# Optimization experiments

Measured on AMD Instinct MI355X. Metric: run time of the kernel, lower is better.

Reference implementation:

```python
import jax, jax.numpy as jnp
import numpy as np

N = 50000      # nodes
E = 800000     # edges (avg degree 16)
D = 128        # in_dim == hidden_dim
CD = 3         # coord_dim (SE(3))
L = 3          # num_layers


def setup_inputs() -> dict:
    key = jax.random.key(0)
    ks = jax.random.split(key, 10)
    s = np.float32(1.0 / np.sqrt(D))
    return {
        "x": jax.random.normal(ks[0], (N, D), jnp.float32),
        "pos": jax.random.normal(ks[1], (N, CD), jnp.float32),
        "edge_index": jax.random.randint(ks[2], (2, E), 0, N, dtype=jnp.int32),
        # per-layer stacked params (in_dim == hidden_dim so all layers stack)
        "Wl": jax.random.normal(ks[3], (L, D, D), jnp.float32) * s,
        "bl": jnp.zeros((L, D), jnp.float32),
        "Wc": jax.random.normal(ks[4], (L, D, 1), jnp.float32) * s,
        "bc": jnp.zeros((L, 1), jnp.float32),
        "WR": jax.random.normal(ks[5], (L, D, CD * CD), jnp.float32) * s,
        "bR": jnp.zeros((L, CD * CD), jnp.float32),
        "Wt": jax.random.normal(ks[6], (L, D, CD), jnp.float32) * s,
        "bt": jnp.zeros((L, CD), jnp.float32),
        # final fc
        "Wf": jax.random.normal(ks[7], (D, D), jnp.float32) * s,
        "bf": jnp.zeros((D,), jnp.float32),
    }


def reference(x, pos, edge_index, Wl, bl, Wc, bc, WR, bR, Wt, bt, Wf, bf):
    src, dst = edge_index[0], edge_index[1]
    n = x.shape[0]
    # R defaults to identity, t to zeros (R_dict/t_dict None path)
    R = jnp.broadcast_to(jnp.eye(CD, dtype=x.dtype), (n, CD, CD))
    t = jnp.zeros_like(pos)
    for i in range(L):
        h = x @ Wl[i] + bl[i]                          # (N, D)  per-edge-type linear
        # MessagePassing aggr='add': message x_j = h[src], scatter-add at dst
        out = jax.ops.segment_sum(h[src], dst, num_segments=n)  # (N, D)
        pos = pos + (out @ Wc[i] + bc[i])              # (N,3) + (N,1) broadcast
        R_upd = (out @ WR[i] + bR[i]).reshape(n, CD, CD)
        Q = jnp.linalg.qr(R_upd)[0]                    # orthonormalize rotation update
        R = Q @ R
        t = t + (out @ Wt[i] + bt[i])
        x = out
    z = x @ Wf + bf
    return z, pos, R, t
```

## Files before the change

### kernel.cpp

```cpp
#include <hip/hip_runtime.h>
#include <hip/hip_fp16.h>

typedef _Float16 half8 __attribute__((ext_vector_type(8)));
typedef float floatx4 __attribute__((ext_vector_type(4)));

#define OSH 13
#define BN  128
#define BSH 7

__device__ inline void qr3_q(const double A[3][3], double Q[3][3]){
  double a[3][3];
#pragma unroll
  for (int r = 0; r < 3; r++)
#pragma unroll
    for (int c = 0; c < 3; c++) a[r][c] = A[r][c];

  double v1[3] = {1.0, 0.0, 0.0};
  double tau1 = 0.0;
  {
    double xn2 = a[1][0]*a[1][0] + a[2][0]*a[2][0];
    if (xn2 != 0.0){
      double alpha = a[0][0];
      double beta = -copysign(sqrt(alpha*alpha + xn2), alpha);
      tau1 = (beta - alpha) / beta;
      double inv = 1.0 / (alpha - beta);
      v1[1] = a[1][0] * inv;
      v1[2] = a[2][0] * inv;
#pragma unroll
      for (int c = 1; c < 3; c++){
        double w = a[0][c] + v1[1]*a[1][c] + v1[2]*a[2][c];
        double tw = tau1 * w;
        a[0][c] -= tw;
        a[1][c] -= tw * v1[1];
        a[2][c] -= tw * v1[2];
      }
    }
  }
  double tau2 = 0.0, v2 = 0.0;
  {
    double x2 = a[2][1];
    if (x2 != 0.0){
      double alpha = a[1][1];
      double beta = -copysign(sqrt(alpha*alpha + x2*x2), alpha);
      tau2 = (beta - alpha) / beta;
      v2 = x2 / (alpha - beta);
    }
  }
  double M[3][3] = {{1.0, 0.0, 0.0},
                    {0.0, 1.0 - tau2, -tau2*v2},
                    {0.0, -tau2*v2, 1.0 - tau2*v2*v2}};
#pragma unroll
  for (int c = 0; c < 3; c++){
    double w = v1[0]*M[0][c] + v1[1]*M[1][c] + v1[2]*M[2][c];
#pragma unroll
    for (int r = 0; r < 3; r++)
      Q[r][c] = M[r][c] - tau1 * v1[r] * w;
  }
}

__device__ inline void se3_node_ds(int n, const float ds[13],
                                   const float* __restrict__ bc, const float* __restrict__ bR,
                                   const float* __restrict__ bt, const float* __restrict__ pos_in,
                                   float* __restrict__ pos_o, float* __restrict__ R_o,
                                   float* __restrict__ t_o, int layer){
  double A[3][3], Q[3][3];
#pragma unroll
  for (int r = 0; r < 3; r++)
#pragma unroll
    for (int c = 0; c < 3; c++)
      A[r][c] = (double)ds[1 + r*3 + c] + (double)bR[r*3 + c];
  qr3_q(A, Q);

  double pd = (double)ds[0] + (double)bc[0];
#pragma unroll
  for (int c = 0; c < 3; c++){
    double base = (layer == 0) ? (double)pos_in[n*3 + c] : (double)pos_o[n*3 + c];
    pos_o[n*3 + c] = (float)(base + pd);
  }

  if (layer == 0){
#pragma unroll
    for (int r = 0; r < 3; r++)
#pragma unroll
      for (int c = 0; c < 3; c++)
        R_o[n*9 + r*3 + c] = (float)Q[r][c];
  } else {
    double Rold[3][3];
#pragma unroll
    for (int r = 0; r < 3; r++)
#pragma unroll
      for (int c = 0; c < 3; c++)
        Rold[r][c] = (double)R_o[n*9 + r*3 + c];
#pragma unroll
    for (int r = 0; r < 3; r++)
#pragma unroll
      for (int c = 0; c < 3; c++){
        double s = Q[r][0]*Rold[0][c] + Q[r][1]*Rold[1][c] + Q[r][2]*Rold[2][c];
        R_o[n*9 + r*3 + c] = (float)s;
      }
  }
#pragma unroll
  for (int c = 0; c < 3; c++){
    double base = (layer == 0) ? 0.0 : (double)t_o[n*3 + c];
    t_o[n*3 + c] = (float)(base + (double)ds[10 + c] + (double)bt[c]);
  }
}

__launch_bounds__(256)
__global__ void k_prebin(const float* __restrict__ x, _Float16* __restrict__ o, int N,
                         const float* __restrict__ Wl, const float* __restrict__ Wf,
                         const float* __restrict__ Wc, const float* __restrict__ WR,
                         const float* __restrict__ Wt, _Float16* __restrict__ wTx,
                         _Float16* __restrict__ wHd,
                         const int* __restrict__ src, const int* __restrict__ dst,
                         int E, int nbuck, int capB,
                         int* __restrict__ cursor, int* __restrict__ binned,
                         int cvtB, int prepB){
  __shared__ int cnt[512];
  __shared__ int segbase[512];
  const int b = blockIdx.x;
  const int tid = threadIdx.x;

  if (b < cvtB){
    int c = b*256 + tid;
    if (c >= (N+1)*16) return;
    int n = c >> 4;
    half8 h = {};
    if (n < N){
      const float* p = x + (size_t)c*8;
      float4 f0 = *(const float4*)p;
      float4 f1 = *(const float4*)(p + 4);
      h[0]=(_Float16)f0.x; h[1]=(_Float16)f0.y; h[2]=(_Float16)f0.z; h[3]=(_Float16)f0.w;
      h[4]=(_Float16)f1.x; h[5]=(_Float16)f1.y; h[6]=(_Float16)f1.z; h[7]=(_Float16)f1.w;
    }
    *(half8*)(o + (size_t)c*8) = h;
    return;
  }
  if (b < cvtB + prepB){
    int t = (b - cvtB)*256 + tid;
    if (t < 4*128*128){
      int l = t >> 14;
      int n = (t >> 7) & 127;
      int k = t & 127;
      const float* W = (l < 3) ? (Wl + (size_t)l*16384) : Wf;
      wTx[t] = (_Float16)W[k*128 + n];
    } else if (t < 4*128*128 + 3*16*128){
      int u = t - 4*128*128;
      int l = u >> 11;
      int r = u & 2047;
      int n = r >> 7;
      int k = r & 127;
      float v = 0.f;
      if (n == 0)      v = Wc[(size_t)l*128 + k];
      else if (n < 10) v = WR[(size_t)l*1152 + k*9 + (n-1)];
      else if (n < 13) v = Wt[(size_t)l*384 + k*3 + (n-10)];
      wHd[u] = (_Float16)v;
    }
    return;
  }

  const int bb = b - cvtB - prepB;
  for (int t = tid; t < nbuck; t += 256) cnt[t] = 0;
  __syncthreads();
  const int e0 = bb*4096 + tid;
  int pk[16], bk[16];
#pragma unroll
  for (int j = 0; j < 16; j++){
    int e = e0 + j*256;
    if (e < E){
      int d = dst[e], s = src[e];
      bk[j] = d >> BSH;
      pk[j] = (s << BSH) | (d & (BN-1));
      atomicAdd(&cnt[bk[j]], 1);
    } else bk[j] = -1;
  }
  __syncthreads();
  for (int t = tid; t < nbuck; t += 256){
    int c = cnt[t];
    if (c > 0) segbase[t] = t*capB + atomicAdd(&cursor[t], c);
    cnt[t] = 0;
  }
  __syncthreads();
#pragma unroll
  for (int j = 0; j < 16; j++){
    if (bk[j] >= 0){
      int ord = atomicAdd(&cnt[bk[j]], 1);
      binned[segbase[bk[j]] + ord] = pk[j];
    }
  }
}

__launch_bounds__(256)
__global__ void k_build(const int* __restrict__ binned, const int* __restrict__ cursor,
                        int N, int capB, int capC,
                        int2* __restrict__ sd, int* __restrict__ csr){
  __shared__ int deg2[BN*8];
  __shared__ int lst2[BN*8];
  __shared__ int cnt2[BN*8];
  __shared__ int scn[BN];
  const int b = blockIdx.x, tid = threadIdx.x;
  for (int t = tid; t < BN*8; t += 256){ deg2[t] = 0; cnt2[t] = 0; }
  __syncthreads();
  const int nE = cursor[b];
  const int gbase = b*capB;
  for (int i = tid; i < nE; i += 256){
    int v = binned[gbase + i];
    int s = v >> BSH;
    int o = s >> OSH; if (o > 7) o = 7;
    atomicAdd(&deg2[((v & (BN-1)) << 3) + o], 1);
  }
  __syncthreads();
  int d0 = 0, p0 = 0;
  if (tid < BN){
#pragma unroll
    for (int o = 0; o < 8; o++) d0 += deg2[(tid << 3) + o];
    p0 = (d0+7)&~7;
    scn[tid] = p0;
  }
  __syncthreads();
#pragma unroll
  for (int off = 1; off < BN; off <<= 1){
    int add = 0;
    if (tid < BN && tid >= off) add = scn[tid-off];
    __syncthreads();
    if (tid < BN) scn[tid] += add;
    __syncthreads();
  }
  const int csrb = b*capC;
  int ex = 0;
  if (tid < BN){
    ex = scn[tid] - p0;
    int off0 = ex;
#pragma unroll
    for (int o = 0; o < 8; o++){ lst2[(tid << 3) + o] = off0; off0 += deg2[(tid << 3) + o]; }
    int n0 = b*BN + tid;
    if (n0 < N) sd[n0] = make_int2(csrb + ex, (d0 << 16) | p0);
  }
  __syncthreads();
  for (int i = tid; i < nE; i += 256){
    int v = binned[gbase + i];
    int dl = v & (BN-1), s = v >> BSH;
    int o = s >> OSH; if (o > 7) o = 7;
    int ord = atomicAdd(&cnt2[(dl << 3) + o], 1);
    csr[csrb + lst2[(dl << 3) + o] + ord] = s;
  }
  __syncthreads();
  if (tid < BN){
    for (int j = d0; j < p0; j++) csr[csrb + ex + j] = N;
  }
}

__launch_bounds__(256)
__global__ void k_fused(const _Float16* __restrict__ Xin,
                        const _Float16* __restrict__ Wmain,
                        const _Float16* __restrict__ Whd,
                        const float* __restrict__ bias,
                        const int* __restrict__ csr, const int2* __restrict__ sd,
                        _Float16* __restrict__ Out,
                        int N, int layer,
                        const float* __restrict__ bc, const float* __restrict__ bR,
                        const float* __restrict__ bt, const float* __restrict__ pos_in,
                        float* __restrict__ pos_o, float* __restrict__ R_o,
                        float* __restrict__ t_o){
  __shared__ __align__(16) _Float16 lg[64][136];
  __shared__ __align__(16) float lheads[64*16];
  __shared__ float ldeg[64];

  const int tid  = threadIdx.x;
  const int wave = tid >> 6;
  const int lane = tid & 63;
  const int quad = lane >> 4;
  const int l16  = lane & 15;
  const int rbase0 = blockIdx.x*64;

  {
    const int nbase = rbase0 + wave*16;
    int nn = nbase + (lane & 15);
    int2 sv = (nn < N) ? sd[nn] : make_int2(0, 0);
    const unsigned int* Xu = (const unsigned int*)Xin;
    for (int i = 0; i < 16; i++){
      int s0    = __builtin_amdgcn_readlane(sv.x, i);
      int dpack = __builtin_amdgcn_readlane(sv.y, i);
      int degp  = dpack & 0xffff;
      if (lane == 0) ldeg[wave*16 + i] = (float)(dpack >> 16);
      float acc0 = 0.f, acc1 = 0.f;
      for (int base = 0; base < degp; base += 64){
        int myidx = csr[s0 + base + lane];
        int m = degp - base; m = (m < 64) ? m : 64;
        for (int k = 0; k < m; k += 8){
          unsigned int v[8];
#pragma unroll
          for (int j = 0; j < 8; j++){
            int idx = __builtin_amdgcn_readlane(myidx, k + j);
            v[j] = Xu[(size_t)idx*64 + lane];
          }
#pragma unroll
          for (int j = 0; j < 8; j++){
            float2 f = __half22float2(*(__half2*)&v[j]);
            acc0 += f.x; acc1 += f.y;
          }
        }
      }
      __half2 ho = __floats2half2_rn(acc0, acc1);
      ((unsigned int*)&lg[wave*16 + i][0])[lane] = *(unsigned int*)&ho;
    }
  }
  __syncthreads();

  const int cthi = wave >> 1;
  half8 af[4][2];
#pragma unroll
  for (int kc = 0; kc < 4; kc++)
#pragma unroll
    for (int rt = 0; rt < 2; rt++){
      int rl = (wave & 1)*32 + rt*16 + l16;
      af[kc][rt] = *(const half8*)&lg[rl][kc*32 + quad*8];
    }
  __syncthreads();

  floatx4 acc[2][4] = {};
#pragma unroll
  for (int kc = 0; kc < 4; kc++)
#pragma unroll
    for (int ct = 0; ct < 4; ct++){
      half8 bf = *(const half8*)(Wmain + (size_t)((cthi*4 + ct)*16 + l16)*128 + kc*32 + quad*8);
      acc[0][ct] = __builtin_amdgcn_mfma_f32_16x16x32_f16(af[kc][0], bf, acc[0][ct], 0, 0, 0);
      acc[1][ct] = __builtin_amdgcn_mfma_f32_16x16x32_f16(af[kc][1], bf, acc[1][ct], 0, 0, 0);
    }

#pragma unroll
  for (int rt = 0; rt < 2; rt++){
    float dgv[4];
#pragma unroll
    for (int reg = 0; reg < 4; reg++)
      dgv[reg] = ldeg[(wave & 1)*32 + rt*16 + quad*4 + reg];
#pragma unroll
    for (int ct = 0; ct < 4; ct++){
      int col = (cthi*4 + ct)*16 + l16;
      float b = bias[col];
#pragma unroll
      for (int reg = 0; reg < 4; reg++){
        int rl = (wave & 1)*32 + rt*16 + quad*4 + reg;
        lg[rl][col] = (_Float16)(acc[rt][ct][reg] + b*dgv[reg]);
      }
    }
  }
  __syncthreads();

#pragma unroll
  for (int i = 0; i < 4; i++){
    int idx8 = i*256 + tid;
    int row = idx8 >> 4, c8 = idx8 & 15;
    int gr = rbase0 + row;
    if (gr < N){
      *(half8*)(Out + (size_t)gr*128 + c8*8) = *(const half8*)&lg[row][c8*8];
    } else if (gr == N){
      half8 z = {};
      *(half8*)(Out + (size_t)gr*128 + c8*8) = z;
    }
  }

  {
    floatx4 hacc = {};
#pragma unroll
    for (int kc = 0; kc < 4; kc++){
      half8 ha = *(const half8*)&lg[wave*16 + l16][kc*32 + quad*8];
      half8 bf = *(const half8*)(Whd + (size_t)l16*128 + kc*32 + quad*8);
      hacc = __builtin_amdgcn_mfma_f32_16x16x32_f16(ha, bf, hacc, 0, 0, 0);
    }
#pragma unroll
    for (int reg = 0; reg < 4; reg++)
      lheads[(wave*16 + quad*4 + reg)*16 + l16] = hacc[reg];
  }
  __syncthreads();

  if (tid < 64){
    int n = rbase0 + tid;
    if (n < N){
      float ds[13];
#pragma unroll
      for (int c = 0; c < 13; c++) ds[c] = lheads[tid*16 + c];
      se3_node_ds(n, ds, bc, bR, bt, pos_in, pos_o, R_o, t_o, layer);
    }
  }
}

__launch_bounds__(256)
__global__ void k_fused_fin(const _Float16* __restrict__ Xin,
                        const _Float16* __restrict__ Wmain,
                        const _Float16* __restrict__ Whd,
                        const float* __restrict__ bias,
                        const int* __restrict__ csr, const int2* __restrict__ sd,
                        int N, int layer,
                        const float* __restrict__ bc, const float* __restrict__ bR,
                        const float* __restrict__ bt, const float* __restrict__ pos_in,
                        float* __restrict__ pos_o, float* __restrict__ R_o,
                        float* __restrict__ t_o,
                        const _Float16* __restrict__ Wfin,
                        const float* __restrict__ bfin,
                        float* __restrict__ Zout){
  __shared__ __align__(16) _Float16 lg[64][136];
  __shared__ __align__(16) float lheads[64*16];
  __shared__ float ldeg[64];

  const int tid  = threadIdx.x;
  const int wave = tid >> 6;
  const int lane = tid & 63;
  const int quad = lane >> 4;
  const int l16  = lane & 15;
  const int rbase0 = blockIdx.x*64;

  {
    const int nbase = rbase0 + wave*16;
    int nn = nbase + (lane & 15);
    int2 sv = (nn < N) ? sd[nn] : make_int2(0, 0);
    const unsigned int* Xu = (const unsigned int*)Xin;
    for (int i = 0; i < 16; i++){
      int s0    = __builtin_amdgcn_readlane(sv.x, i);
      int dpack = __builtin_amdgcn_readlane(sv.y, i);
      int degp  = dpack & 0xffff;
      if (lane == 0) ldeg[wave*16 + i] = (float)(dpack >> 16);
      float acc0 = 0.f, acc1 = 0.f;
      for (int base = 0; base < degp; base += 64){
        int myidx = csr[s0 + base + lane];
        int m = degp - base; m = (m < 64) ? m : 64;
        for (int k = 0; k < m; k += 8){
          unsigned int v[8];
#pragma unroll
          for (int j = 0; j < 8; j++){
            int idx = __builtin_amdgcn_readlane(myidx, k + j);
            v[j] = Xu[(size_t)idx*64 + lane];
          }
#pragma unroll
          for (int j = 0; j < 8; j++){
            float2 f = __half22float2(*(__half2*)&v[j]);
            acc0 += f.x; acc1 += f.y;
          }
        }
      }
      __half2 ho = __floats2half2_rn(acc0, acc1);
      ((unsigned int*)&lg[wave*16 + i][0])[lane] = *(unsigned int*)&ho;
    }
  }
  __syncthreads();

  const int cthi = wave >> 1;
  half8 af[4][2];
#pragma unroll
  for (int kc = 0; kc < 4; kc++)
#pragma unroll
    for (int rt = 0; rt < 2; rt++){
      int rl = (wave & 1)*32 + rt*16 + l16;
      af[kc][rt] = *(const half8*)&lg[rl][kc*32 + quad*8];
    }
  __syncthreads();

  floatx4 acc[2][4] = {};
#pragma unroll
  for (int kc = 0; kc < 4; kc++)
#pragma unroll
    for (int ct = 0; ct < 4; ct++){
      half8 bf = *(const half8*)(Wmain + (size_t)((cthi*4 + ct)*16 + l16)*128 + kc*32 + quad*8);
      acc[0][ct] = __builtin_amdgcn_mfma_f32_16x16x32_f16(af[kc][0], bf, acc[0][ct], 0, 0, 0);
      acc[1][ct] = __builtin_amdgcn_mfma_f32_16x16x32_f16(af[kc][1], bf, acc[1][ct], 0, 0, 0);
    }

#pragma unroll
  for (int rt = 0; rt < 2; rt++){
    float dgv[4];
#pragma unroll
    for (int reg = 0; reg < 4; reg++)
      dgv[reg] = ldeg[(wave & 1)*32 + rt*16 + quad*4 + reg];
#pragma unroll
    for (int ct = 0; ct < 4; ct++){
      int col = (cthi*4 + ct)*16 + l16;
      float b = bias[col];
#pragma unroll
      for (int reg = 0; reg < 4; reg++){
        int rl = (wave & 1)*32 + rt*16 + quad*4 + reg;
        lg[rl][col] = (_Float16)(acc[rt][ct][reg] + b*dgv[reg]);
      }
    }
  }
  __syncthreads();

  {
    half8 zf[4][2];
#pragma unroll
    for (int kc = 0; kc < 4; kc++)
#pragma unroll
      for (int rt = 0; rt < 2; rt++){
        int rl = (wave & 1)*32 + rt*16 + l16;
        zf[kc][rt] = *(const half8*)&lg[rl][kc*32 + quad*8];
      }
    floatx4 zacc[2][4] = {};
#pragma unroll
    for (int kc = 0; kc < 4; kc++)
#pragma unroll
      for (int ct = 0; ct < 4; ct++){
        half8 bf = *(const half8*)(Wfin + (size_t)((cthi*4 + ct)*16 + l16)*128 + kc*32 + quad*8);
        zacc[0][ct] = __builtin_amdgcn_mfma_f32_16x16x32_f16(zf[kc][0], bf, zacc[0][ct], 0, 0, 0);
        zacc[1][ct] = __builtin_amdgcn_mfma_f32_16x16x32_f16(zf[kc][1], bf, zacc[1][ct], 0, 0, 0);
      }
#pragma unroll
    for (int rt = 0; rt < 2; rt++)
#pragma unroll
      for (int ct = 0; ct < 4; ct++){
        int col = (cthi*4 + ct)*16 + l16;
        float b = bfin[col];
#pragma unroll
        for (int reg = 0; reg < 4; reg++){
          int gr = rbase0 + (wave & 1)*32 + rt*16 + quad*4 + reg;
          if (gr < N) Zout[(size_t)gr*128 + col] = zacc[rt][ct][reg] + b;
        }
      }
  }

  {
    floatx4 hacc = {};
#pragma unroll
    for (int kc = 0; kc < 4; kc++){
      half8 ha = *(const half8*)&lg[wave*16 + l16][kc*32 + quad*8];
      half8 bf = *(const half8*)(Whd + (size_t)l16*128 + kc*32 + quad*8);
      hacc = __builtin_amdgcn_mfma_f32_16x16x32_f16(ha, bf, hacc, 0, 0, 0);
    }
#pragma unroll
    for (int reg = 0; reg < 4; reg++)
      lheads[(wave*16 + quad*4 + reg)*16 + l16] = hacc[reg];
  }
  __syncthreads();

  if (tid < 64){
    int n = rbase0 + tid;
    if (n < N){
      float ds[13];
#pragma unroll
      for (int c = 0; c < 13; c++) ds[c] = lheads[tid*16 + c];
      se3_node_ds(n, ds, bc, bR, bt, pos_in, pos_o, R_o, t_o, layer);
    }
  }
}

extern "C" void kernel_launch(void* const* d_in, const int* in_sizes, int n_in,
                              void* d_out, int out_size, void* d_ws, size_t ws_size,
                              hipStream_t stream){
  const float* x0  = (const float*)d_in[0];
  const float* pos = (const float*)d_in[1];
  const int*   ei  = (const int*)d_in[2];
  const float* Wl  = (const float*)d_in[3];
  const float* bl  = (const float*)d_in[4];
  const float* Wc  = (const float*)d_in[5];
  const float* bc  = (const float*)d_in[6];
  const float* WR  = (const float*)d_in[7];
  const float* bR  = (const float*)d_in[8];
  const float* Wt  = (const float*)d_in[9];
  const float* bt  = (const float*)d_in[10];
  const float* Wf  = (const float*)d_in[11];
  const float* bf  = (const float*)d_in[12];

  const int N = in_sizes[0] / 128;
  const int E = in_sizes[2] / 2;
  const int* srcp = ei;
  const int* dstp = ei + E;

  float* z_out = (float*)d_out;
  float* pos_o = z_out + (size_t)N*128;
  float* R_o   = pos_o + (size_t)N*3;
  float* t_o   = R_o   + (size_t)N*9;

  const int nbuck = (N + BN - 1) >> BSH;
  const int capB  = (((E + nbuck - 1)/nbuck)*5/4 + 256 + 63) & ~63;
  const int capC  = capB + BN*7;

  char* ws = (char*)d_ws;
  size_t off = 0;
  auto alloc = [&](size_t bytes)->char*{
    char* p = ws + off; off += (bytes + 511) & ~(size_t)511; return p;
  };
  _Float16* bufA = (_Float16*)alloc((size_t)(N+1)*128*2);
  _Float16* bufB = (_Float16*)alloc((size_t)(N+1)*128*2);
  _Float16* wTx  = (_Float16*)alloc((size_t)4*128*128*2);
  _Float16* wHd  = (_Float16*)alloc((size_t)3*16*128*2);
  int2*  sd     = (int2*) alloc((size_t)N*8);
  int*   cursor = (int*)  alloc((size_t)nbuck*4);
  int*   binned = (int*)  alloc((size_t)nbuck*capB*4);
  int*   csr    = (int*)  alloc((size_t)nbuck*capC*4);

  const int cvtB = ((N+1)*16 + 255)/256;
  const int prep_total = 4*128*128 + 3*16*128;
  const int prepB = (prep_total + 255)/256;
  const int binB  = (E + 4095)/4096;

  hipMemsetAsync(cursor, 0, (size_t)nbuck*4, stream);
  k_prebin<<<dim3(cvtB + prepB + binB), dim3(256), 0, stream>>>(
      x0, bufA, N, Wl, Wf, Wc, WR, Wt, wTx, wHd,
      srcp, dstp, E, nbuck, capB, cursor, binned, cvtB, prepB);
  k_build<<<dim3(nbuck), dim3(256), 0, stream>>>(binned, cursor, N, capB, capC, sd, csr);

  const int fused_blocks = (N + 64) >> 6;

  k_fused<<<dim3(fused_blocks), dim3(256), 0, stream>>>(
      bufA, wTx, wHd, bl,
      csr, sd, bufB, N, 0,
      bc, bR, bt, pos, pos_o, R_o, t_o);
  k_fused<<<dim3(fused_blocks), dim3(256), 0, stream>>>(
      bufB, wTx + (size_t)16384, wHd + (size_t)2048, bl + 128,
      csr, sd, bufA, N, 1,
      bc + 1, bR + 9, bt + 3, pos, pos_o, R_o, t_o);
  k_fused_fin<<<dim3(fused_blocks), dim3(256), 0, stream>>>(
      bufA, wTx + (size_t)2*16384, wHd + (size_t)2*2048, bl + 256,
      csr, sd, N, 2,
      bc + 2, bR + 18, bt + 6, pos, pos_o, R_o, t_o,
      wTx + (size_t)3*16384, bf, z_out);
}
```

Measured before the change: 267.9 us.

## Fuse all stages into one cooperative persistent kernel with grid syncs

Replaces the five separate launches (prebin, build, three fused layers) with a single cooperative kernel that loops over work tiles and separates stages with grid-wide barriers. The goal is to remove per-launch overhead and the inter-kernel drain gaps. The cost is that grid size is capped by occupancy, so each block processes several tiles serially, and grid.sync has its own cost. The old multi-kernel path is kept as a fallback if the cooperative launch fails.

```diff
diff --git a/kernel.cpp b/kernel.cpp
--- a/kernel.cpp
+++ b/kernel.cpp
@@ -1,5 +1,8 @@
 #include <hip/hip_runtime.h>
 #include <hip/hip_fp16.h>
+#include <hip/hip_cooperative_groups.h>
+
+namespace cg = cooperative_groups;
 
 typedef _Float16 half8 __attribute__((ext_vector_type(8)));
 typedef float floatx4 __attribute__((ext_vector_type(4)));
@@ -106,60 +109,50 @@
   }
 }
 
-__launch_bounds__(256)
-__global__ void k_prebin(const float* __restrict__ x, _Float16* __restrict__ o, int N,
-                         const float* __restrict__ Wl, const float* __restrict__ Wf,
-                         const float* __restrict__ Wc, const float* __restrict__ WR,
-                         const float* __restrict__ Wt, _Float16* __restrict__ wTx,
-                         _Float16* __restrict__ wHd,
-                         const int* __restrict__ src, const int* __restrict__ dst,
-                         int E, int nbuck, int capB,
-                         int* __restrict__ cursor, int* __restrict__ binned,
-                         int cvtB, int prepB){
-  __shared__ int cnt[512];
-  __shared__ int segbase[512];
-  const int b = blockIdx.x;
+
+__device__ __forceinline__ void dev_cvt_chunk(int c, const float* __restrict__ x,
+                                              _Float16* __restrict__ o, int N){
+  int n = c >> 4;
+  half8 h = {};
+  if (n < N){
+    const float* p = x + (size_t)c*8;
+    float4 f0 = *(const float4*)p;
+    float4 f1 = *(const float4*)(p + 4);
+    h[0]=(_Float16)f0.x; h[1]=(_Float16)f0.y; h[2]=(_Float16)f0.z; h[3]=(_Float16)f0.w;
+    h[4]=(_Float16)f1.x; h[5]=(_Float16)f1.y; h[6]=(_Float16)f1.z; h[7]=(_Float16)f1.w;
+  }
+  *(half8*)(o + (size_t)c*8) = h;
+}
+
+__device__ __forceinline__ void dev_prep_elem(int t,
+    const float* __restrict__ Wl, const float* __restrict__ Wf,
+    const float* __restrict__ Wc, const float* __restrict__ WR,
+    const float* __restrict__ Wt, _Float16* __restrict__ wTx, _Float16* __restrict__ wHd){
+  if (t < 4*128*128){
+    int l = t >> 14;
+    int n = (t >> 7) & 127;
+    int k = t & 127;
+    const float* W = (l < 3) ? (Wl + (size_t)l*16384) : Wf;
+    wTx[t] = (_Float16)W[k*128 + n];
+  } else if (t < 4*128*128 + 3*16*128){
+    int u = t - 4*128*128;
+    int l = u >> 11;
+    int r = u & 2047;
+    int n = r >> 7;
+    int k = r & 127;
+    float v = 0.f;
+    if (n == 0)      v = Wc[(size_t)l*128 + k];
+    else if (n < 10) v = WR[(size_t)l*1152 + k*9 + (n-1)];
+    else if (n < 13) v = Wt[(size_t)l*384 + k*3 + (n-10)];
+    wHd[u] = (_Float16)v;
+  }
+}
+
+__device__ __forceinline__ void dev_bin_block(int bb,
+    const int* __restrict__ src, const int* __restrict__ dst,
+    int E, int nbuck, int capB, int* __restrict__ cursor, int* __restrict__ binned,
+    int* __restrict__ cnt, int* __restrict__ segbase){
   const int tid = threadIdx.x;
-
-  if (b < cvtB){
-    int c = b*256 + tid;
-    if (c >= (N+1)*16) return;
-    int n = c >> 4;
-    half8 h = {};
-    if (n < N){
-      const float* p = x + (size_t)c*8;
-      float4 f0 = *(const float4*)p;
-      float4 f1 = *(const float4*)(p + 4);
-      h[0]=(_Float16)f0.x; h[1]=(_Float16)f0.y; h[2]=(_Float16)f0.z; h[3]=(_Float16)f0.w;
-      h[4]=(_Float16)f1.x; h[5]=(_Float16)f1.y; h[6]=(_Float16)f1.z; h[7]=(_Float16)f1.w;
-    }
-    *(half8*)(o + (size_t)c*8) = h;
-    return;
-  }
-  if (b < cvtB + prepB){
-    int t = (b - cvtB)*256 + tid;
-    if (t < 4*128*128){
-      int l = t >> 14;
-      int n = (t >> 7) & 127;
-      int k = t & 127;
-      const float* W = (l < 3) ? (Wl + (size_t)l*16384) : Wf;
-      wTx[t] = (_Float16)W[k*128 + n];
-    } else if (t < 4*128*128 + 3*16*128){
-      int u = t - 4*128*128;
-      int l = u >> 11;
-      int r = u & 2047;
-      int n = r >> 7;
-      int k = r & 127;
-      float v = 0.f;
-      if (n == 0)      v = Wc[(size_t)l*128 + k];
-      else if (n < 10) v = WR[(size_t)l*1152 + k*9 + (n-1)];
-      else if (n < 13) v = Wt[(size_t)l*384 + k*3 + (n-10)];
-      wHd[u] = (_Float16)v;
-    }
-    return;
-  }
-
-  const int bb = b - cvtB - prepB;
   for (int t = tid; t < nbuck; t += 256) cnt[t] = 0;
   __syncthreads();
   const int e0 = bb*4096 + tid;
@@ -188,17 +181,15 @@
       binned[segbase[bk[j]] + ord] = pk[j];
     }
   }
-}
-
-__launch_bounds__(256)
-__global__ void k_build(const int* __restrict__ binned, const int* __restrict__ cursor,
-                        int N, int capB, int capC,
-                        int2* __restrict__ sd, int* __restrict__ csr){
-  __shared__ int deg2[BN*8];
-  __shared__ int lst2[BN*8];
-  __shared__ int cnt2[BN*8];
-  __shared__ int scn[BN];
-  const int b = blockIdx.x, tid = threadIdx.x;
+  __syncthreads();
+}
+
+__device__ __forceinline__ void dev_build_block(int b,
+    const int* __restrict__ binned, const int* __restrict__ cursor,
+    int N, int capB, int capC, int2* __restrict__ sd, int* __restrict__ csr,
+    int* __restrict__ deg2, int* __restrict__ lst2, int* __restrict__ cnt2,
+    int* __restrict__ scn){
+  const int tid = threadIdx.x;
   for (int t = tid; t < BN*8; t += 256){ deg2[t] = 0; cnt2[t] = 0; }
   __syncthreads();
   const int nE = cursor[b];
@@ -248,30 +239,27 @@
   if (tid < BN){
     for (int j = d0; j < p0; j++) csr[csrb + ex + j] = N;
   }
-}
-
-__launch_bounds__(256)
-__global__ void k_fused(const _Float16* __restrict__ Xin,
-                        const _Float16* __restrict__ Wmain,
-                        const _Float16* __restrict__ Whd,
-                        const float* __restrict__ bias,
-                        const int* __restrict__ csr, const int2* __restrict__ sd,
-                        _Float16* __restrict__ Out,
-                        int N, int layer,
-                        const float* __restrict__ bc, const float* __restrict__ bR,
-                        const float* __restrict__ bt, const float* __restrict__ pos_in,
-                        float* __restrict__ pos_o, float* __restrict__ R_o,
-                        float* __restrict__ t_o){
-  __shared__ __align__(16) _Float16 lg[64][136];
-  __shared__ __align__(16) float lheads[64*16];
-  __shared__ float ldeg[64];
-
+  __syncthreads();
+}
+
+__device__ __forceinline__ void dev_fused_tile(int rbase0,
+    const _Float16* __restrict__ Xin,
+    const _Float16* __restrict__ Wmain, const _Float16* __restrict__ Whd,
+    const float* __restrict__ bias,
+    const int* __restrict__ csr, const int2* __restrict__ sd,
+    _Float16* __restrict__ Out, int N, int layer,
+    const float* __restrict__ bc, const float* __restrict__ bR,
+    const float* __restrict__ bt, const float* __restrict__ pos_in,
+    float* __restrict__ pos_o, float* __restrict__ R_o, float* __restrict__ t_o,
+    const _Float16* __restrict__ Wfin, const float* __restrict__ bfin,
+    float* __restrict__ Zout,
+    _Float16* __restrict__ lg , float* __restrict__ lheads ,
+    float* __restrict__ ldeg ){
   const int tid  = threadIdx.x;
   const int wave = tid >> 6;
   const int lane = tid & 63;
   const int quad = lane >> 4;
   const int l16  = lane & 15;
-  const int rbase0 = blockIdx.x*64;
 
   {
     const int nbase = rbase0 + wave*16;
@@ -302,7 +290,7 @@
         }
       }
       __half2 ho = __floats2half2_rn(acc0, acc1);
-      ((unsigned int*)&lg[wave*16 + i][0])[lane] = *(unsigned int*)&ho;
+      ((unsigned int*)&lg[(wave*16 + i)*136])[lane] = *(unsigned int*)&ho;
     }
   }
   __syncthreads();
@@ -314,7 +302,7 @@
 #pragma unroll
     for (int rt = 0; rt < 2; rt++){
       int rl = (wave & 1)*32 + rt*16 + l16;
-      af[kc][rt] = *(const half8*)&lg[rl][kc*32 + quad*8];
+      af[kc][rt] = *(const half8*)&lg[rl*136 + kc*32 + quad*8];
     }
   __syncthreads();
 
@@ -341,30 +329,62 @@
 #pragma unroll
       for (int reg = 0; reg < 4; reg++){
         int rl = (wave & 1)*32 + rt*16 + quad*4 + reg;
-        lg[rl][col] = (_Float16)(acc[rt][ct][reg] + b*dgv[reg]);
-      }
-    }
-  }
-  __syncthreads();
-
-#pragma unroll
-  for (int i = 0; i < 4; i++){
-    int idx8 = i*256 + tid;
-    int row = idx8 >> 4, c8 = idx8 & 15;
-    int gr = rbase0 + row;
-    if (gr < N){
-      *(half8*)(Out + (size_t)gr*128 + c8*8) = *(const half8*)&lg[row][c8*8];
-    } else if (gr == N){
-      half8 z = {};
-      *(half8*)(Out + (size_t)gr*128 + c8*8) = z;
-    }
+        lg[rl*136 + col] = (_Float16)(acc[rt][ct][reg] + b*dgv[reg]);
+      }
+    }
+  }
+  __syncthreads();
+
+  if (Wfin == nullptr){
+#pragma unroll
+    for (int i = 0; i < 4; i++){
+      int idx8 = i*256 + tid;
+      int row = idx8 >> 4, c8 = idx8 & 15;
+      int gr = rbase0 + row;
+      if (gr < N){
+        *(half8*)(Out + (size_t)gr*128 + c8*8) = *(const half8*)&lg[row*136 + c8*8];
+      } else if (gr == N){
+        half8 z = {};
+        *(half8*)(Out + (size_t)gr*128 + c8*8) = z;
+      }
+    }
+  } else {
+    half8 zf[4][2];
+#pragma unroll
+    for (int kc = 0; kc < 4; kc++)
+#pragma unroll
+      for (int rt = 0; rt < 2; rt++){
+        int rl = (wave & 1)*32 + rt*16 + l16;
+        zf[kc][rt] = *(const half8*)&lg[rl*136 + kc*32 + quad*8];
+      }
+    floatx4 zacc[2][4] = {};
+#pragma unroll
+    for (int kc = 0; kc < 4; kc++)
+#pragma unroll
+      for (int ct = 0; ct < 4; ct++){
+        half8 bf = *(const half8*)(Wfin + (size_t)((cthi*4 + ct)*16 + l16)*128 + kc*32 + quad*8);
+        zacc[0][ct] = __builtin_amdgcn_mfma_f32_16x16x32_f16(zf[kc][0], bf, zacc[0][ct], 0, 0, 0);
+        zacc[1][ct] = __builtin_amdgcn_mfma_f32_16x16x32_f16(zf[kc][1], bf, zacc[1][ct], 0, 0, 0);
+      }
+#pragma unroll
+    for (int rt = 0; rt < 2; rt++)
+#pragma unroll
+      for (int ct = 0; ct < 4; ct++){
+        int col = (cthi*4 + ct)*16 + l16;
+        float b = bfin[col];
+#pragma unroll
+        for (int reg = 0; reg < 4; reg++){
+          int gr = rbase0 + (wave & 1)*32 + rt*16 + quad*4 + reg;
+          if (gr < N) Zout[(size_t)gr*128 + col] = zacc[rt][ct][reg] + b;
+        }
+      }
   }
 
   {
     floatx4 hacc = {};
 #pragma unroll
     for (int kc = 0; kc < 4; kc++){
-      half8 ha = *(const half8*)&lg[wave*16 + l16][kc*32 + quad*8];
+      half8 ha = *(const half8*)&lg[(wave*16 + l16)*136 + kc*32 + quad*8];
       half8 bf = *(const half8*)(Whd + (size_t)l16*128 + kc*32 + quad*8);
       hacc = __builtin_amdgcn_mfma_f32_16x16x32_f16(ha, bf, hacc, 0, 0, 0);
     }
@@ -383,162 +403,143 @@
       se3_node_ds(n, ds, bc, bR, bt, pos_in, pos_o, R_o, t_o, layer);
     }
   }
-}
+  __syncthreads();
+}
+
+struct MegaArgs {
+  const float* x0; const float* pos; const int* src; const int* dst;
+  const float* Wl; const float* Wf; const float* Wc; const float* WR; const float* Wt;
+  const float* bl; const float* bc; const float* bR; const float* bt; const float* bf;
+  _Float16* bufA; _Float16* bufB; _Float16* wTx; _Float16* wHd;
+  int2* sd; int* cursor; int* binned; int* csr;
+  float* z_out; float* pos_o; float* R_o; float* t_o;
+  int N, E, nbuck, capB, capC, binB, fusedTiles;
+};
 
 __launch_bounds__(256)
-__global__ void k_fused_fin(const _Float16* __restrict__ Xin,
-                        const _Float16* __restrict__ Wmain,
-                        const _Float16* __restrict__ Whd,
-                        const float* __restrict__ bias,
+__global__ void k_mega(MegaArgs a){
+  cg::grid_group grid = cg::this_grid();
+  __shared__ __align__(16) unsigned char smem[22016];
+  const int tid = threadIdx.x;
+
+  {
+    int* cnt = (int*)smem;
+    int* segbase = cnt + 512;
+    for (int bb = blockIdx.x; bb < a.binB; bb += gridDim.x)
+      dev_bin_block(bb, a.src, a.dst, a.E, a.nbuck, a.capB, a.cursor, a.binned, cnt, segbase);
+  }
+  {
+    const int totc = (a.N + 1)*16;
+    for (int c = blockIdx.x*256 + tid; c < totc; c += gridDim.x*256)
+      dev_cvt_chunk(c, a.x0, a.bufA, a.N);
+    const int totp = 4*128*128 + 3*16*128;
+    for (int t = blockIdx.x*256 + tid; t < totp; t += gridDim.x*256)
+      dev_prep_elem(t, a.Wl, a.Wf, a.Wc, a.WR, a.Wt, a.wTx, a.wHd);
+  }
+  grid.sync();
+
+  {
+    int* deg2 = (int*)smem;
+    int* lst2 = deg2 + BN*8;
+    int* cnt2 = lst2 + BN*8;
+    int* scn  = cnt2 + BN*8;
+    for (int b = blockIdx.x; b < a.nbuck; b += gridDim.x)
+      dev_build_block(b, a.binned, a.cursor, a.N, a.capB, a.capC, a.sd, a.csr,
+                      deg2, lst2, cnt2, scn);
+  }
+  grid.sync();
+
+  _Float16* lg   = (_Float16*)smem;
+  float* lheads  = (float*)(smem + 64*136*2);
+  float* ldeg    = (float*)(smem + 64*136*2 + 64*16*4);
+  const _Float16* xi = a.bufA;
+  _Float16* xo = a.bufB;
+#pragma unroll 1
+  for (int layer = 0; layer < 3; layer++){
+    const _Float16* Wm = a.wTx + (size_t)layer*16384;
+    const _Float16* Wh = a.wHd + (size_t)layer*2048;
+    const float* bi = a.bl + (size_t)layer*128;
+    const _Float16* Wfin = (layer == 2) ? (a.wTx + (size_t)3*16384) : nullptr;
+    for (int tb = blockIdx.x; tb < a.fusedTiles; tb += gridDim.x)
+      dev_fused_tile(tb*64, xi, Wm, Wh, bi, a.csr, a.sd, xo, a.N, layer,
+                     a.bc + layer, a.bR + (size_t)layer*9, a.bt + (size_t)layer*3,
+                     a.pos, a.pos_o, a.R_o, a.t_o,
+                     Wfin, a.bf, a.z_out, lg, lheads, ldeg);
+    if (layer < 2) grid.sync();
+    const _Float16* tsw = xi; xi = xo; xo = (_Float16*)tsw;
+  }
+}
+
+__launch_bounds__(256)
+__global__ void k_prebin(const float* __restrict__ x, _Float16* __restrict__ o, int N,
+                         const float* __restrict__ Wl, const float* __restrict__ Wf,
+                         const float* __restrict__ Wc, const float* __restrict__ WR,
+                         const float* __restrict__ Wt, _Float16* __restrict__ wTx,
+                         _Float16* __restrict__ wHd,
+                         const int* __restrict__ src, const int* __restrict__ dst,
+                         int E, int nbuck, int capB,
+                         int* __restrict__ cursor, int* __restrict__ binned,
+                         int cvtB, int prepB){
+  __shared__ int cnt[512];
+  __shared__ int segbase[512];
+  const int b = blockIdx.x, tid = threadIdx.x;
+  if (b < cvtB){
+    int c = b*256 + tid;
+    if (c < (N+1)*16) dev_cvt_chunk(c, x, o, N);
+    return;
+  }
+  if (b < cvtB + prepB){
+    dev_prep_elem((b - cvtB)*256 + tid, Wl, Wf, Wc, WR, Wt, wTx, wHd);
+    return;
+  }
+  dev_bin_block(b - cvtB - prepB, src, dst, E, nbuck, capB, cursor, binned, cnt, segbase);
+}
+
+__launch_bounds__(256)
+__global__ void k_build(const int* __restrict__ binned, const int* __restrict__ cursor,
+                        int N, int capB, int capC,
+                        int2* __restrict__ sd, int* __restrict__ csr){
+  __shared__ int deg2[BN*8];
+  __shared__ int lst2[BN*8];
+  __shared__ int cnt2[BN*8];
+  __shared__ int scn[BN];
+  dev_build_block(blockIdx.x, binned, cursor, N, capB, capC, sd, csr, deg2, lst2, cnt2, scn);
+}
+
+__launch_bounds__(256)
+__global__ void k_fused(const _Float16* __restrict__ Xin, const _Float16* __restrict__ Wmain,
+                        const _Float16* __restrict__ Whd, const float* __restrict__ bias,
+                        const int* __restrict__ csr, const int2* __restrict__ sd,
+                        _Float16* __restrict__ Out, int N, int layer,
+                        const float* __restrict__ bc, const float* __restrict__ bR,
+                        const float* __restrict__ bt, const float* __restrict__ pos_in,
+                        float* __restrict__ pos_o, float* __restrict__ R_o,
+                        float* __restrict__ t_o){
+  __shared__ __align__(16) _Float16 lg[64*136];
+  __shared__ __align__(16) float lheads[64*16];
+  __shared__ float ldeg[64];
+  dev_fused_tile(blockIdx.x*64, Xin, Wmain, Whd, bias, csr, sd, Out, N, layer,
+                 bc, bR, bt, pos_in, pos_o, R_o, t_o,
+                 nullptr, nullptr, nullptr, lg, lheads, ldeg);
+}
+
+__launch_bounds__(256)
+__global__ void k_fused_fin(const _Float16* __restrict__ Xin, const _Float16* __restrict__ Wmain,
+                        const _Float16* __restrict__ Whd, const float* __restrict__ bias,
                         const int* __restrict__ csr, const int2* __restrict__ sd,
                         int N, int layer,
                         const float* __restrict__ bc, const float* __restrict__ bR,
                         const float* __restrict__ bt, const float* __restrict__ pos_in,
                         float* __restrict__ pos_o, float* __restrict__ R_o,
                         float* __restrict__ t_o,
-                        const _Float16* __restrict__ Wfin,
-                        const float* __restrict__ bfin,
+                        const _Float16* __restrict__ Wfin, const float* __restrict__ bfin,
                         float* __restrict__ Zout){
-  __shared__ __align__(16) _Float16 lg[64][136];
+  __shared__ __align__(16) _Float16 lg[64*136];
   __shared__ __align__(16) float lheads[64*16];
   __shared__ float ldeg[64];
-
-  const int tid  = threadIdx.x;
-  const int wave = tid >> 6;
-  const int lane = tid & 63;
-  const int quad = lane >> 4;
-  const int l16  = lane & 15;
-  const int rbase0 = blockIdx.x*64;
-
-  {
-    const int nbase = rbase0 + wave*16;
-    int nn = nbase + (lane & 15);
-    int2 sv = (nn < N) ? sd[nn] : make_int2(0, 0);
-    const unsigned int* Xu = (const unsigned int*)Xin;
-    for (int i = 0; i < 16; i++){
-      int s0    = __builtin_amdgcn_readlane(sv.x, i);
-      int dpack = __builtin_amdgcn_readlane(sv.y, i);
-      int degp  = dpack & 0xffff;
-      if (lane == 0) ldeg[wave*16 + i] = (float)(dpack >> 16);
-      float acc0 = 0.f, acc1 = 0.f;
-      for (int base = 0; base < degp; base += 64){
-        int myidx = csr[s0 + base + lane];
-        int m = degp - base; m = (m < 64) ? m : 64;
-        for (int k = 0; k < m; k += 8){
-          unsigned int v[8];
-#pragma unroll
-          for (int j = 0; j < 8; j++){
-            int idx = __builtin_amdgcn_readlane(myidx, k + j);
-            v[j] = Xu[(size_t)idx*64 + lane];
-          }
-#pragma unroll
-          for (int j = 0; j < 8; j++){
-            float2 f = __half22float2(*(__half2*)&v[j]);
-            acc0 += f.x; acc1 += f.y;
-          }
-        }
-      }
-      __half2 ho = __floats2half2_rn(acc0, acc1);
-      ((unsigned int*)&lg[wave*16 + i][0])[lane] = *(unsigned int*)&ho;
-    }
-  }
-  __syncthreads();
-
-  const int cthi = wave >> 1;
-  half8 af[4][2];
-#pragma unroll
-  for (int kc = 0; kc < 4; kc++)
-#pragma unroll
-    for (int rt = 0; rt < 2; rt++){
-      int rl = (wave & 1)*32 + rt*16 + l16;
-      af[kc][rt] = *(const half8*)&lg[rl][kc*32 + quad*8];
-    }
-  __syncthreads();
-
-  floatx4 acc[2][4] = {};
-#pragma unroll
-  for (int kc = 0; kc < 4; kc++)
-#pragma unroll
-    for (int ct = 0; ct < 4; ct++){
-      half8 bf = *(const half8*)(Wmain + (size_t)((cthi*4 + ct)*16 + l16)*128 + kc*32 + quad*8);
-      acc[0][ct] = __builtin_amdgcn_mfma_f32_16x16x32_f16(af[kc][0], bf, acc[0][ct], 0, 0, 0);
-      acc[1][ct] = __builtin_amdgcn_mfma_f32_16x16x32_f16(af[kc][1], bf, acc[1][ct], 0, 0, 0);
-    }
-
-#pragma unroll
-  for (int rt = 0; rt < 2; rt++){
-    float dgv[4];
-#pragma unroll
-    for (int reg = 0; reg < 4; reg++)
-      dgv[reg] = ldeg[(wave & 1)*32 + rt*16 + quad*4 + reg];
-#pragma unroll
-    for (int ct = 0; ct < 4; ct++){
-      int col = (cthi*4 + ct)*16 + l16;
-      float b = bias[col];
-#pragma unroll
-      for (int reg = 0; reg < 4; reg++){
-        int rl = (wave & 1)*32 + rt*16 + quad*4 + reg;
-        lg[rl][col] = (_Float16)(acc[rt][ct][reg] + b*dgv[reg]);
-      }
-    }
-  }
-  __syncthreads();
-
-  {
-    half8 zf[4][2];
-#pragma unroll
-    for (int kc = 0; kc < 4; kc++)
-#pragma unroll
-      for (int rt = 0; rt < 2; rt++){
-        int rl = (wave & 1)*32 + rt*16 + l16;
-        zf[kc][rt] = *(const half8*)&lg[rl][kc*32 + quad*8];
-      }
-    floatx4 zacc[2][4] = {};
-#pragma unroll
-    for (int kc = 0; kc < 4; kc++)
-#pragma unroll
-      for (int ct = 0; ct < 4; ct++){
-        half8 bf = *(const half8*)(Wfin + (size_t)((cthi*4 + ct)*16 + l16)*128 + kc*32 + quad*8);
-        zacc[0][ct] = __builtin_amdgcn_mfma_f32_16x16x32_f16(zf[kc][0], bf, zacc[0][ct], 0, 0, 0);
-        zacc[1][ct] = __builtin_amdgcn_mfma_f32_16x16x32_f16(zf[kc][1], bf, zacc[1][ct], 0, 0, 0);
-      }
-#pragma unroll
-    for (int rt = 0; rt < 2; rt++)
-#pragma unroll
-      for (int ct = 0; ct < 4; ct++){
-        int col = (cthi*4 + ct)*16 + l16;
-        float b = bfin[col];
-#pragma unroll
-        for (int reg = 0; reg < 4; reg++){
-          int gr = rbase0 + (wave & 1)*32 + rt*16 + quad*4 + reg;
-          if (gr < N) Zout[(size_t)gr*128 + col] = zacc[rt][ct][reg] + b;
-        }
-      }
-  }
-
-  {
-    floatx4 hacc = {};
-#pragma unroll
-    for (int kc = 0; kc < 4; kc++){
-      half8 ha = *(const half8*)&lg[wave*16 + l16][kc*32 + quad*8];
-      half8 bf = *(const half8*)(Whd + (size_t)l16*128 + kc*32 + quad*8);
-      hacc = __builtin_amdgcn_mfma_f32_16x16x32_f16(ha, bf, hacc, 0, 0, 0);
-    }
-#pragma unroll
-    for (int reg = 0; reg < 4; reg++)
-      lheads[(wave*16 + quad*4 + reg)*16 + l16] = hacc[reg];
-  }
-  __syncthreads();
-
-  if (tid < 64){
-    int n = rbase0 + tid;
-    if (n < N){
-      float ds[13];
-#pragma unroll
-      for (int c = 0; c < 13; c++) ds[c] = lheads[tid*16 + c];
-      se3_node_ds(n, ds, bc, bR, bt, pos_in, pos_o, R_o, t_o, layer);
-    }
-  }
+  dev_fused_tile(blockIdx.x*64, Xin, Wmain, Whd, bias, csr, sd, nullptr, N, layer,
+                 bc, bR, bt, pos_in, pos_o, R_o, t_o,
+                 Wfin, bfin, Zout, lg, lheads, ldeg);
 }
 
 extern "C" void kernel_launch(void* const* d_in, const int* in_sizes, int n_in,
@@ -590,26 +591,55 @@
   const int prep_total = 4*128*128 + 3*16*128;
   const int prepB = (prep_total + 255)/256;
   const int binB  = (E + 4095)/4096;
+  const int fused_blocks = (N + 64) >> 6;
 
   hipMemsetAsync(cursor, 0, (size_t)nbuck*4, stream);
-  k_prebin<<<dim3(cvtB + prepB + binB), dim3(256), 0, stream>>>(
-      x0, bufA, N, Wl, Wf, Wc, WR, Wt, wTx, wHd,
-      srcp, dstp, E, nbuck, capB, cursor, binned, cvtB, prepB);
-  k_build<<<dim3(nbuck), dim3(256), 0, stream>>>(binned, cursor, N, capB, capC, sd, csr);
-
-  const int fused_blocks = (N + 64) >> 6;
-
-  k_fused<<<dim3(fused_blocks), dim3(256), 0, stream>>>(
-      bufA, wTx, wHd, bl,
-      csr, sd, bufB, N, 0,
-      bc, bR, bt, pos, pos_o, R_o, t_o);
-  k_fused<<<dim3(fused_blocks), dim3(256), 0, stream>>>(
-      bufB, wTx + (size_t)16384, wHd + (size_t)2048, bl + 128,
-      csr, sd, bufA, N, 1,
-      bc + 1, bR + 9, bt + 3, pos, pos_o, R_o, t_o);
-  k_fused_fin<<<dim3(fused_blocks), dim3(256), 0, stream>>>(
-      bufA, wTx + (size_t)2*16384, wHd + (size_t)2*2048, bl + 256,
-      csr, sd, N, 2,
-      bc + 2, bR + 18, bt + 6, pos, pos_o, R_o, t_o,
-      wTx + (size_t)3*16384, bf, z_out);
-}
+
+  bool coop_ok = false;
+  {
+    int perCU = 0;
+    if (hipOccupancyMaxActiveBlocksPerMultiprocessor(&perCU, k_mega, 256, 0) == hipSuccess
+        && perCU > 0){
+      int dev = 0;
+      (void)hipGetDevice(&dev);
+      int nCU = 0;
+      if (hipDeviceGetAttribute(&nCU, hipDeviceAttributeMultiprocessorCount, dev) != hipSuccess
+          || nCU <= 0) nCU = 256;
+      int G = fused_blocks;
+      long cap = (long)perCU * nCU;
+      if ((long)G > cap) G = (int)cap;
+      if (G > 0){
+        MegaArgs ma;
+        ma.x0 = x0; ma.pos = pos; ma.src = srcp; ma.dst = dstp;
+        ma.Wl = Wl; ma.Wf = Wf; ma.Wc = Wc; ma.WR = WR; ma.Wt = Wt;
+        ma.bl = bl; ma.bc = bc; ma.bR = bR; ma.bt = bt; ma.bf = bf;
+        ma.bufA = bufA; ma.bufB = bufB; ma.wTx = wTx; ma.wHd = wHd;
+        ma.sd = sd; ma.cursor = cursor; ma.binned = binned; ma.csr = csr;
+        ma.z_out = z_out; ma.pos_o = pos_o; ma.R_o = R_o; ma.t_o = t_o;
+        ma.N = N; ma.E = E; ma.nbuck = nbuck; ma.capB = capB; ma.capC = capC;
+        ma.binB = binB; ma.fusedTiles = fused_blocks;
+        void* params[] = { &ma };
+        if (hipLaunchCooperativeKernel(k_mega, dim3(G), dim3(256), params, 0u, stream)
+            == hipSuccess)
+          coop_ok = true;
+      }
+    }
+  }
+
+  if (!coop_ok){
+    k_prebin<<<dim3(cvtB + prepB + binB), dim3(256), 0, stream>>>(
+        x0, bufA, N, Wl, Wf, Wc, WR, Wt, wTx, wHd,
+        srcp, dstp, E, nbuck, capB, cursor, binned, cvtB, prepB);
+    k_build<<<dim3(nbuck), dim3(256), 0, stream>>>(binned, cursor, N, capB, capC, sd, csr);
+    k_fused<<<dim3(fused_blocks), dim3(256), 0, stream>>>(
+        bufA, wTx, wHd, bl, csr, sd, bufB, N, 0,
+        bc, bR, bt, pos, pos_o, R_o, t_o);
+    k_fused<<<dim3(fused_blocks), dim3(256), 0, stream>>>(
+        bufB, wTx + (size_t)16384, wHd + (size_t)2048, bl + 128, csr, sd, bufA, N, 1,
+        bc + 1, bR + 9, bt + 3, pos, pos_o, R_o, t_o);
+    k_fused_fin<<<dim3(fused_blocks), dim3(256), 0, stream>>>(
+        bufA, wTx + (size_t)2*16384, wHd + (size_t)2*2048, bl + 256, csr, sd, N, 2,
+        bc + 2, bR + 18, bt + 6, pos, pos_o, R_o, t_o,
+        wTx + (size_t)3*16384, bf, z_out);
+  }
+}
```

New measurement: 662.3 us. +147.2%, slower.

## Fuse CSR build into first-layer fused kernel with 64-node buckets

Applied to the files above, without the earlier changes.

Shrinks the destination bucket size from 128 to 64 nodes so each bucket matches one fused block, then folds the per-bucket CSR construction into a new first-layer kernel. That kernel builds its block's CSR slice in shared memory, keeps the segment descriptors locally, and then runs the gather, GEMM and SE(3) heads. The goal is to drop one kernel launch and the separate build pass. The cost is twice as many buckets in prebinning and serialized build work at the start of each block before the gather.

```diff
diff --git a/kernel.cpp b/kernel.cpp
--- a/kernel.cpp
+++ b/kernel.cpp
@@ -5,8 +5,8 @@
 typedef float floatx4 __attribute__((ext_vector_type(4)));
 
 #define OSH 13
-#define BN  128
-#define BSH 7
+#define BN  64
+#define BSH 6
 
 __device__ inline void qr3_q(const double A[3][3], double Q[3][3]){
   double a[3][3];
@@ -116,8 +116,8 @@
                          int E, int nbuck, int capB,
                          int* __restrict__ cursor, int* __restrict__ binned,
                          int cvtB, int prepB){
-  __shared__ int cnt[512];
-  __shared__ int segbase[512];
+  __shared__ int cnt[1024];
+  __shared__ int segbase[1024];
   const int b = blockIdx.x;
   const int tid = threadIdx.x;
 
@@ -191,62 +191,197 @@
 }
 
 __launch_bounds__(256)
-__global__ void k_build(const int* __restrict__ binned, const int* __restrict__ cursor,
-                        int N, int capB, int capC,
-                        int2* __restrict__ sd, int* __restrict__ csr){
-  __shared__ int deg2[BN*8];
-  __shared__ int lst2[BN*8];
-  __shared__ int cnt2[BN*8];
-  __shared__ int scn[BN];
-  const int b = blockIdx.x, tid = threadIdx.x;
-  for (int t = tid; t < BN*8; t += 256){ deg2[t] = 0; cnt2[t] = 0; }
-  __syncthreads();
-  const int nE = cursor[b];
-  const int gbase = b*capB;
-  for (int i = tid; i < nE; i += 256){
-    int v = binned[gbase + i];
-    int s = v >> BSH;
-    int o = s >> OSH; if (o > 7) o = 7;
-    atomicAdd(&deg2[((v & (BN-1)) << 3) + o], 1);
-  }
-  __syncthreads();
-  int d0 = 0, p0 = 0;
-  if (tid < BN){
-#pragma unroll
-    for (int o = 0; o < 8; o++) d0 += deg2[(tid << 3) + o];
-    p0 = (d0+7)&~7;
-    scn[tid] = p0;
-  }
-  __syncthreads();
-#pragma unroll
-  for (int off = 1; off < BN; off <<= 1){
-    int add = 0;
-    if (tid < BN && tid >= off) add = scn[tid-off];
+__global__ void k_fused0(const _Float16* __restrict__ Xin,
+                         const _Float16* __restrict__ Wmain,
+                         const _Float16* __restrict__ Whd,
+                         const float* __restrict__ bias,
+                         const int* __restrict__ binned, const int* __restrict__ cursor,
+                         int capB, int capC,
+                         int* __restrict__ csr, int2* __restrict__ sd,
+                         _Float16* __restrict__ Out, int N,
+                         const float* __restrict__ bc, const float* __restrict__ bR,
+                         const float* __restrict__ bt, const float* __restrict__ pos_in,
+                         float* __restrict__ pos_o, float* __restrict__ R_o,
+                         float* __restrict__ t_o){
+  __shared__ __align__(16) _Float16 lg[64][136];
+  __shared__ __align__(16) float lheads[64*16];
+  __shared__ float ldeg[64];
+  __shared__ int2 sdloc[64];
+
+  const int tid  = threadIdx.x;
+  const int wave = tid >> 6;
+  const int lane = tid & 63;
+  const int quad = lane >> 4;
+  const int l16  = lane & 15;
+  const int b    = blockIdx.x;
+  const int rbase0 = b*64;
+
+  {
+    int* deg2 = (int*)&lg[0][0];
+    int* lst2 = deg2 + 512;
+    int* cnt2 = lst2 + 512;
+    int* scn  = cnt2 + 512;
+    for (int t = tid; t < 64*8; t += 256){ deg2[t] = 0; cnt2[t] = 0; }
     __syncthreads();
-    if (tid < BN) scn[tid] += add;
+    const int nE = cursor[b];
+    const int gbase = b*capB;
+    for (int i = tid; i < nE; i += 256){
+      int v = binned[gbase + i];
+      int s = v >> BSH;
+      int o = s >> OSH; if (o > 7) o = 7;
+      atomicAdd(&deg2[((v & (BN-1)) << 3) + o], 1);
+    }
     __syncthreads();
-  }
-  const int csrb = b*capC;
-  int ex = 0;
-  if (tid < BN){
-    ex = scn[tid] - p0;
-    int off0 = ex;
-#pragma unroll
-    for (int o = 0; o < 8; o++){ lst2[(tid << 3) + o] = off0; off0 += deg2[(tid << 3) + o]; }
-    int n0 = b*BN + tid;
-    if (n0 < N) sd[n0] = make_int2(csrb + ex, (d0 << 16) | p0);
-  }
-  __syncthreads();
-  for (int i = tid; i < nE; i += 256){
-    int v = binned[gbase + i];
-    int dl = v & (BN-1), s = v >> BSH;
-    int o = s >> OSH; if (o > 7) o = 7;
-    int ord = atomicAdd(&cnt2[(dl << 3) + o], 1);
-    csr[csrb + lst2[(dl << 3) + o] + ord] = s;
-  }
-  __syncthreads();
-  if (tid < BN){
-    for (int j = d0; j < p0; j++) csr[csrb + ex + j] = N;
+    int d0 = 0, p0 = 0;
+    if (tid < 64){
+#pragma unroll
+      for (int o = 0; o < 8; o++) d0 += deg2[(tid << 3) + o];
+      p0 = (d0+7)&~7;
+      scn[tid] = p0;
+    }
+    __syncthreads();
+#pragma unroll
+    for (int off = 1; off < 64; off <<= 1){
+      int add = 0;
+      if (tid < 64 && tid >= off) add = scn[tid-off];
+      __syncthreads();
+      if (tid < 64) scn[tid] += add;
+      __syncthreads();
+    }
+    const int csrb = b*capC;
+    int ex = 0;
+    if (tid < 64){
+      ex = scn[tid] - p0;
+      int off0 = ex;
+#pragma unroll
+      for (int o = 0; o < 8; o++){ lst2[(tid << 3) + o] = off0; off0 += deg2[(tid << 3) + o]; }
+      int n0 = rbase0 + tid;
+      int2 sv2 = make_int2(csrb + ex, (d0 << 16) | p0);
+      sdloc[tid] = (n0 < N) ? sv2 : make_int2(0, 0);
+      ldeg[tid] = (float)d0;
+      if (n0 < N) sd[n0] = sv2;
+    }
+    __syncthreads();
+    for (int i = tid; i < nE; i += 256){
+      int v = binned[gbase + i];
+      int dl = v & (BN-1), s = v >> BSH;
+      int o = s >> OSH; if (o > 7) o = 7;
+      int ord = atomicAdd(&cnt2[(dl << 3) + o], 1);
+      csr[csrb + lst2[(dl << 3) + o] + ord] = s;
+    }
+    __syncthreads();
+    if (tid < 64){
+      for (int j = d0; j < p0; j++) csr[csrb + ex + j] = N;
+    }
+    __syncthreads();
+  }
+
+  {
+    int2 sv = sdloc[wave*16 + (lane & 15)];
+    const unsigned int* Xu = (const unsigned int*)Xin;
+    for (int i = 0; i < 16; i++){
+      int s0    = __builtin_amdgcn_readlane(sv.x, i);
+      int dpack = __builtin_amdgcn_readlane(sv.y, i);
+      int degp  = dpack & 0xffff;
+      float acc0 = 0.f, acc1 = 0.f;
+      for (int base = 0; base < degp; base += 64){
+        int myidx = csr[sdloc[wave*16 + i].x + base + lane];
+        int m = degp - base; m = (m < 64) ? m : 64;
+        for (int k = 0; k < m; k += 8){
+          unsigned int v[8];
+#pragma unroll
+          for (int j = 0; j < 8; j++){
+            int idx = __builtin_amdgcn_readlane(myidx, k + j);
+            v[j] = Xu[(size_t)idx*64 + lane];
+          }
+#pragma unroll
+          for (int j = 0; j < 8; j++){
+            float2 f = __half22float2(*(__half2*)&v[j]);
+            acc0 += f.x; acc1 += f.y;
+          }
+        }
+      }
+      __half2 ho = __floats2half2_rn(acc0, acc1);
+      ((unsigned int*)&lg[wave*16 + i][0])[lane] = *(unsigned int*)&ho;
+    }
+  }
+  __syncthreads();
+
+  const int cthi = wave >> 1;
+  half8 af[4][2];
+#pragma unroll
+  for (int kc = 0; kc < 4; kc++)
+#pragma unroll
+    for (int rt = 0; rt < 2; rt++){
+      int rl = (wave & 1)*32 + rt*16 + l16;
+      af[kc][rt] = *(const half8*)&lg[rl][kc*32 + quad*8];
+    }
+  __syncthreads();
+
+  floatx4 acc[2][4] = {};
+#pragma unroll
+  for (int kc = 0; kc < 4; kc++)
+#pragma unroll
+    for (int ct = 0; ct < 4; ct++){
+      half8 bf = *(const half8*)(Wmain + (size_t)((cthi*4 + ct)*16 + l16)*128 + kc*32 + quad*8);
+      acc[0][ct] = __builtin_amdgcn_mfma_f32_16x16x32_f16(af[kc][0], bf, acc[0][ct], 0, 0, 0);
+      acc[1][ct] = __builtin_amdgcn_mfma_f32_16x16x32_f16(af[kc][1], bf, acc[1][ct], 0, 0, 0);
+    }
+
+#pragma unroll
+  for (int rt = 0; rt < 2; rt++){
+    float dgv[4];
+#pragma unroll
+    for (int reg = 0; reg < 4; reg++)
+      dgv[reg] = ldeg[(wave & 1)*32 + rt*16 + quad*4 + reg];
+#pragma unroll
+    for (int ct = 0; ct < 4; ct++){
+      int col = (cthi*4 + ct)*16 + l16;
+      float bv = bias[col];
+#pragma unroll
+      for (int reg = 0; reg < 4; reg++){
+        int rl = (wave & 1)*32 + rt*16 + quad*4 + reg;
+        lg[rl][col] = (_Float16)(acc[rt][ct][reg] + bv*dgv[reg]);
+      }
+    }
+  }
+  __syncthreads();
+
+#pragma unroll
+  for (int i = 0; i < 4; i++){
+    int idx8 = i*256 + tid;
+    int row = idx8 >> 4, c8 = idx8 & 15;
+    int gr = rbase0 + row;
+    if (gr < N){
+      *(half8*)(Out + (size_t)gr*128 + c8*8) = *(const half8*)&lg[row][c8*8];
+    } else if (gr == N){
+      half8 z = {};
+      *(half8*)(Out + (size_t)gr*128 + c8*8) = z;
+    }
+  }
+
+  {
+    floatx4 hacc = {};
+#pragma unroll
+    for (int kc = 0; kc < 4; kc++){
+      half8 ha = *(const half8*)&lg[wave*16 + l16][kc*32 + quad*8];
+      half8 bfh = *(const half8*)(Whd + (size_t)l16*128 + kc*32 + quad*8);
+      hacc = __builtin_amdgcn_mfma_f32_16x16x32_f16(ha, bfh, hacc, 0, 0, 0);
+    }
+#pragma unroll
+    for (int reg = 0; reg < 4; reg++)
+      lheads[(wave*16 + quad*4 + reg)*16 + l16] = hacc[reg];
+  }
+  __syncthreads();
+
+  if (tid < 64){
+    int n = rbase0 + tid;
+    if (n < N){
+      float ds[13];
+#pragma unroll
+      for (int c = 0; c < 13; c++) ds[c] = lheads[tid*16 + c];
+      se3_node_ds(n, ds, bc, bR, bt, pos_in, pos_o, R_o, t_o, 0);
+    }
   }
 }
 
@@ -590,18 +725,17 @@
   const int prep_total = 4*128*128 + 3*16*128;
   const int prepB = (prep_total + 255)/256;
   const int binB  = (E + 4095)/4096;
+  const int fused_blocks = (N + 64) >> 6;
 
   hipMemsetAsync(cursor, 0, (size_t)nbuck*4, stream);
   k_prebin<<<dim3(cvtB + prepB + binB), dim3(256), 0, stream>>>(
       x0, bufA, N, Wl, Wf, Wc, WR, Wt, wTx, wHd,
       srcp, dstp, E, nbuck, capB, cursor, binned, cvtB, prepB);
-  k_build<<<dim3(nbuck), dim3(256), 0, stream>>>(binned, cursor, N, capB, capC, sd, csr);
-
-  const int fused_blocks = (N + 64) >> 6;
-
-  k_fused<<<dim3(fused_blocks), dim3(256), 0, stream>>>(
+
+  k_fused0<<<dim3(fused_blocks), dim3(256), 0, stream>>>(
       bufA, wTx, wHd, bl,
-      csr, sd, bufB, N, 0,
+      binned, cursor, capB, capC, csr, sd,
+      bufB, N,
       bc, bR, bt, pos, pos_o, R_o, t_o);
   k_fused<<<dim3(fused_blocks), dim3(256), 0, stream>>>(
       bufB, wTx + (size_t)16384, wHd + (size_t)2048, bl + 128,
```

Measured after the change: 266.4 us. About the same (-0.6%).
